# Performance work log

Hardware: AMD Instinct MI355X
Metric: run time of the kernel (lower is better)

The kernel has to match this reference:

```python
import jax, jax.numpy as jnp
import numpy as np

EPS = 1e-5  # BatchNorm eps

def _bn(x):
    # BatchNorm1d(affine=False) in training mode: per-agent, per-feature batch stats
    m = jnp.mean(x, axis=1, keepdims=True)
    v = jnp.var(x, axis=1, keepdims=True)
    return (x - m) / jnp.sqrt(v + EPS)

def _lrelu(x):
    return jax.nn.leaky_relu(x, 0.01)

def setup_inputs() -> dict:
    key = jax.random.key(0)
    ks = jax.random.split(key, 14)
    A, B, IN, OUT, H, K = 8, 32768, 128, 32, 128, 4
    D = H // K
    s = 0.05
    return {
        "states": jax.random.normal(ks[0], (A, B, IN), jnp.float32),
        "actions": jax.random.normal(ks[1], (A, B, OUT), jnp.float32),
        "enc_w": jax.random.normal(ks[2], (A, IN + OUT, H), jnp.float32) * s,
        "enc_b": jax.random.normal(ks[3], (A, H), jnp.float32) * s,
        "aenc_w": jax.random.normal(ks[4], (A, OUT, H), jnp.float32) * s,
        "aenc_b": jax.random.normal(ks[5], (A, H), jnp.float32) * s,
        "key_w": jax.random.normal(ks[6], (K, H, D), jnp.float32) * s,
        "sel_w": jax.random.normal(ks[7], (K, H, D), jnp.float32) * s,
        "val_w": jax.random.normal(ks[8], (K, H, D), jnp.float32) * s,
        "val_b": jax.random.normal(ks[9], (K, D), jnp.float32) * s,
        "c1_w": jax.random.normal(ks[10], (A, 2 * H, H), jnp.float32) * s,
        "c1_b": jax.random.normal(ks[11], (A, H), jnp.float32) * s,
        "c2_w": jax.random.normal(ks[12], (A, H, 1), jnp.float32) * s,
        "c2_b": jax.random.normal(ks[13], (A, 1), jnp.float32) * s,
    }

def reference(states, actions, enc_w, enc_b, aenc_w, aenc_b,
              key_w, sel_w, val_w, val_b, c1_w, c1_b, c2_w, c2_b):
    A, B, _ = states.shape
    # per-agent state-action encodings: [A,B,H]
    sa = _bn(jnp.concatenate([states, actions], axis=-1))
    sa_enc = _lrelu(jnp.einsum('abi,aih->abh', sa, enc_w) + enc_b[:, None, :])
    # per-agent action encodings: [A,B,H]
    a_in = _bn(actions)
    a_enc = _lrelu(jnp.einsum('abi,aih->abh', a_in, aenc_w) + aenc_b[:, None, :])
    # per-head keys/values/selectors: [K,A,B,D]
    keys = jnp.einsum('abh,khd->kabd', a_enc, key_w)
    vals = _lrelu(jnp.einsum('abh,khd->kabd', a_enc, val_w) + val_b[:, None, None, :])
    sels = jnp.einsum('abh,khd->kabd', sa_enc, sel_w)
    D = keys.shape[-1]
    # attention logits over other agents: [K,B,A_query,A_key], self excluded
    logits = jnp.einsum('kibd,kjbd->kbij', sels, keys) / jnp.sqrt(jnp.float32(D))
    self_mask = jnp.eye(A, dtype=bool)[None, None]
    probs = jax.nn.softmax(jnp.where(self_mask, -jnp.inf, logits), axis=-1)
    # attended values: [K,A,B,D] -> concat heads -> [A,B,K*D]
    other = jnp.einsum('kbij,kjbd->kibd', probs, vals)
    other_cat = jnp.transpose(other, (1, 2, 0, 3)).reshape(A, B, -1)
    # per-agent critics on [sa_enc, attended]: [A,B,1]
    critic_in = jnp.concatenate([sa_enc, other_cat], axis=-1)
    h = _lrelu(jnp.einsum('abi,aih->abh', critic_in, c1_w) + c1_b[:, None, :])
    q = jnp.einsum('abh,aho->abo', h, c2_w) + c2_b[:, None, :]
    return q
```

## Files before the change

kernel.cpp:

```cpp
#include <hip/hip_runtime.h>
#include <hip/hip_bf16.h>
#include <stdint.h>

#define A_N 8
#define B_N 32768
#define IN_N 128
#define OUT_N 32
#define SAF 160
#define H_N 128
#define D_N 32
#define KD_N 128
#define CIN_N 256
#define CHUNKS 128
#define EPSV 1e-5f

typedef unsigned int u32;
typedef unsigned short u16;
typedef __attribute__((ext_vector_type(8))) short short8;
typedef __attribute__((ext_vector_type(4))) float floatx4;

typedef __attribute__((address_space(1))) void gvoid;
typedef __attribute__((address_space(3))) void lvoid;
__device__ __forceinline__ void glds16(const void* g, void* l){
  __builtin_amdgcn_global_load_lds((gvoid*)g, (lvoid*)l, 16, 0, 0);
}

__device__ __forceinline__ float bf_lo(u32 u){ return __uint_as_float(u << 16); }
__device__ __forceinline__ float bf_hi(u32 u){ return __uint_as_float(u & 0xffff0000u); }
__device__ __forceinline__ float bf2f(u16 b){ return __uint_as_float(((u32)b) << 16); }
__device__ __forceinline__ u16 f2bf(float f){
  u32 u = __float_as_uint(f);
  return (u16)((u + 0x7fffu + ((u >> 16) & 1u)) >> 16);
}
__device__ __forceinline__ float lrelu(float x){ return x > 0.f ? x : 0.01f * x; }

__global__ __launch_bounds__(256) void k_stats(
    const float* __restrict__ states, const float* __restrict__ actions,
    float* __restrict__ part)
{
  int a = blockIdx.y;
  int chunk = blockIdx.x;
  int t = threadIdx.x;
  int r0 = chunk * (B_N / CHUNKS);
  __shared__ float red[512];
  {
    int f = t & 127, half = t >> 7;
    const float* p = states + ((size_t)a * B_N + r0 + half) * IN_N + f;
    float s1 = 0.f, s2 = 0.f;
    for (int it = 0; it < 128; ++it){
      float v = p[(size_t)(2 * it) * IN_N];
      s1 += v; s2 += v * v;
    }
    red[t] = s1; red[256 + t] = s2;
    __syncthreads();
    if (t < 128){
      float a1 = red[t] + red[t + 128];
      float a2 = red[256 + t] + red[256 + t + 128];
      size_t o = (((size_t)a * CHUNKS + chunk) * SAF + t) * 2;
      part[o] = a1; part[o + 1] = a2;
    }
    __syncthreads();
  }
  {
    int f = t & 31, g = t >> 5;
    const float* p = actions + ((size_t)a * B_N + r0 + g) * OUT_N + f;
    float s1 = 0.f, s2 = 0.f;
    for (int it = 0; it < 32; ++it){
      float v = p[(size_t)(8 * it) * OUT_N];
      s1 += v; s2 += v * v;
    }
    red[t] = s1; red[256 + t] = s2;
    __syncthreads();
    if (t < 32){
      float a1 = 0.f, a2 = 0.f;
      #pragma unroll
      for (int gg = 0; gg < 8; ++gg){
        a1 += red[t + 32 * gg];
        a2 += red[256 + t + 32 * gg];
      }
      size_t o = (((size_t)a * CHUNKS + chunk) * SAF + 128 + t) * 2;
      part[o] = a1; part[o + 1] = a2;
    }
  }
}

__global__ void k_finalize(const float* __restrict__ part,
                           float* __restrict__ meanArr, float* __restrict__ istdArr)
{
  int idx = blockIdx.x * blockDim.x + threadIdx.x;
  if (idx >= A_N * SAF) return;
  int a = idx / SAF, f = idx % SAF;
  float s1 = 0.f, s2 = 0.f;
  for (int c = 0; c < CHUNKS; ++c){
    size_t o = (((size_t)a * CHUNKS + c) * SAF + f) * 2;
    s1 += part[o]; s2 += part[o + 1];
  }
  float m = s1 * (1.f / B_N);
  float v = s2 * (1.f / B_N) - m * m;
  if (v < 0.f) v = 0.f;
  meanArr[idx] = m;
  istdArr[idx] = rsqrtf(v + EPSV);
}

__device__ __forceinline__ void packpair(float w, u16* __restrict__ dh,
                                         u16* __restrict__ dl, int i){
  u16 h = f2bf(w);
  dh[i] = h;
  dl[i] = f2bf(w - bf2f(h));
}

__global__ __launch_bounds__(256) void k_pack(
    const float* __restrict__ enc_w, const float* __restrict__ aenc_w,
    const float* __restrict__ key_w, const float* __restrict__ sel_w,
    const float* __restrict__ val_w, const float* __restrict__ c1_w,
    u16* __restrict__ encH, u16* __restrict__ encL,
    u16* __restrict__ aencH, u16* __restrict__ aencL,
    u16* __restrict__ keyH, u16* __restrict__ selH, u16* __restrict__ valH,
    u16* __restrict__ c1H, u16* __restrict__ c1L)
{
  int i = blockIdx.x * 256 + threadIdx.x;
  const int S0 = A_N * H_N * SAF;
  const int S1 = A_N * H_N * OUT_N;
  const int S2 = KD_N * H_N;
  const int S5 = A_N * H_N * CIN_N;
  if (i < S0){
    int a = i / (H_N * SAF); int r = i % (H_N * SAF);
    int tile = r >> 12; int rr = r & 4095;
    int n = rr >> 5; int kk = rr & 31;
    int kg = tile * 32 + kk;
    packpair(enc_w[((size_t)a * SAF + kg) * H_N + n], encH, encL, i);
    return;
  }
  i -= S0;
  if (i < S1){
    int a = i >> 12; int rr = i & 4095;
    int n = rr >> 5; int k = rr & 31;
    packpair(aenc_w[((size_t)a * OUT_N + k) * H_N + n], aencH, aencL, i);
    return;
  }
  i -= S1;
  if (i < 3 * S2){
    int which = i / S2; int j = i % S2;
    int tile = j >> 12; int rr = j & 4095;
    int n = rr >> 5; int kk = rr & 31;
    int kg = tile * 32 + kk;
    const float* w = (which == 0) ? key_w : ((which == 1) ? sel_w : val_w);
    u16* dh = (which == 0) ? keyH : ((which == 1) ? selH : valH);
    dh[j] = f2bf(w[(((size_t)(n >> 5)) * H_N + kg) * D_N + (n & 31)]);
    return;
  }
  i -= 3 * S2;
  if (i < S5){
    int a = i >> 15; int r = i & 32767;
    int tile = r >> 12; int rr = r & 4095;
    int n = rr >> 5; int kk = rr & 31;
    int kg = tile * 32 + kk;
    packpair(c1_w[((size_t)a * CIN_N + kg) * H_N + n], c1H, c1L, i);
  }
}
#define PACK_TOTAL (A_N*H_N*SAF + A_N*H_N*OUT_N + 3*KD_N*H_N + A_N*H_N*CIN_N)

__global__ __launch_bounds__(256, 3) void k_enc_sel(
    const float* __restrict__ states, const float* __restrict__ actions,
    const float* __restrict__ mean, const float* __restrict__ istd,
    const u16* __restrict__ encH, const u16* __restrict__ encL,
    const float* __restrict__ enc_b,
    const u16* __restrict__ selH,
    u16* __restrict__ sa_enc, u16* __restrict__ sels)
{
  int a = blockIdx.y; int row0 = blockIdx.x * 128; int t = threadIdx.x;
  int lane = t & 63, wave = t >> 6, l16 = lane & 15, quad = lane >> 4;
  __shared__ __align__(16) u16 S[25600];
  __shared__ __align__(16) float sc[160], sh[160];
  u16* Wh = S;
  u16* Wl = S + 4096;
  u16* Xh = S + 8192;
  u16* Xl = S + 13312;
  u16* T  = S;
  u16* Ws = S + 17408;

  if (t < SAF){
    float m = mean[a * SAF + t], s = istd[a * SAF + t];
    sc[t] = s; sh[t] = -m * s;
  }
  floatx4 acc[2][8];
  #pragma unroll
  for (int mt = 0; mt < 2; ++mt)
    #pragma unroll
    for (int nt = 0; nt < 8; ++nt) acc[mt][nt] = (floatx4){0.f,0.f,0.f,0.f};
  const u16* ebh = encH + (size_t)a * (H_N * SAF);
  const u16* ebl = encL + (size_t)a * (H_N * SAF);
  __syncthreads();

  for (int k0 = 0; k0 < SAF; k0 += 32){
    const u16* th = ebh + (k0 >> 5) * 4096;
    const u16* tl = ebl + (k0 >> 5) * 4096;
    #pragma unroll
    for (int c = t; c < 512; c += 256){
      glds16(th + c * 8, Wh + c * 8);
      glds16(tl + c * 8, Wl + c * 8);
    }
    for (int c = t; c < 1024; c += 256){
      int r = c >> 3, kc = (c & 7) * 4, f = k0 + kc;
      size_t row = (size_t)a * B_N + row0 + r;
      float4 v;
      if (f < IN_N) v = *(const float4*)(states + row * IN_N + f);
      else          v = *(const float4*)(actions + row * OUT_N + (f - IN_N));
      float4 scv = *(const float4*)&sc[f];
      float4 shv = *(const float4*)&sh[f];
      float x0 = fmaf(v.x, scv.x, shv.x), x1 = fmaf(v.y, scv.y, shv.y);
      float x2 = fmaf(v.z, scv.z, shv.z), x3 = fmaf(v.w, scv.w, shv.w);
      u16 h0 = f2bf(x0), h1 = f2bf(x1), h2 = f2bf(x2), h3 = f2bf(x3);
      uint2 hv; hv.x = (u32)h0 | ((u32)h1 << 16); hv.y = (u32)h2 | ((u32)h3 << 16);
      *(uint2*)&Xh[r * 40 + kc] = hv;
      u16 l0 = f2bf(x0 - bf2f(h0)), l1 = f2bf(x1 - bf2f(h1));
      u16 l2 = f2bf(x2 - bf2f(h2)), l3 = f2bf(x3 - bf2f(h3));
      uint2 lv; lv.x = (u32)l0 | ((u32)l1 << 16); lv.y = (u32)l2 | ((u32)l3 << 16);
      *(uint2*)&Xl[r * 40 + kc] = lv;
    }
    __syncthreads();
    {
      short8 ah[2], al[2], bh[8], bl[8];
      #pragma unroll
      for (int mt = 0; mt < 2; ++mt){
        int rr = (wave * 32 + mt * 16 + l16) * 40 + quad * 8;
        ah[mt] = *(const short8*)&Xh[rr];
        al[mt] = *(const short8*)&Xl[rr];
      }
      #pragma unroll
      for (int nt = 0; nt < 8; ++nt){
        int rr = (nt * 16 + l16) * 32 + quad * 8;
        bh[nt] = *(const short8*)&Wh[rr];
        bl[nt] = *(const short8*)&Wl[rr];
      }
      #pragma unroll
      for (int mt = 0; mt < 2; ++mt)
        #pragma unroll
        for (int nt = 0; nt < 8; ++nt){
          acc[mt][nt] = __builtin_amdgcn_mfma_f32_16x16x32_bf16(ah[mt], bh[nt], acc[mt][nt], 0,0,0);
          acc[mt][nt] = __builtin_amdgcn_mfma_f32_16x16x32_bf16(ah[mt], bl[nt], acc[mt][nt], 0,0,0);
          acc[mt][nt] = __builtin_amdgcn_mfma_f32_16x16x32_bf16(al[mt], bh[nt], acc[mt][nt], 0,0,0);
        }
    }
    __syncthreads();
  }

  {
    float bv[8];
    #pragma unroll
    for (int nt = 0; nt < 8; ++nt) bv[nt] = enc_b[a * H_N + nt * 16 + l16];
    #pragma unroll
    for (int mt = 0; mt < 2; ++mt)
      #pragma unroll
      for (int nt = 0; nt < 8; ++nt)
        #pragma unroll
        for (int r = 0; r < 4; ++r){
          int rl = wave * 32 + mt * 16 + quad * 4 + r;
          T[rl * 136 + nt * 16 + l16] = f2bf(lrelu(acc[mt][nt][r] + bv[nt]));
        }
  }
  __syncthreads();
  for (int c = t; c < 2048; c += 256){
    int row = c >> 4, col8 = (c & 15) * 8;
    *(uint4*)(sa_enc + ((size_t)a * B_N + row0 + row) * H_N + col8) =
        *(const uint4*)&T[row * 136 + col8];
  }

  #pragma unroll
  for (int mt = 0; mt < 2; ++mt)
    #pragma unroll
    for (int nt = 0; nt < 8; ++nt) acc[mt][nt] = (floatx4){0.f,0.f,0.f,0.f};
  for (int k0 = 0; k0 < H_N; k0 += 64){
    #pragma unroll
    for (int c = t; c < 1024; c += 256)
      glds16(selH + (k0 >> 5) * 4096 + c * 8, Ws + c * 8);
    __syncthreads();
    #pragma unroll
    for (int ks = 0; ks < 64; ks += 32){
      short8 ah[2], bh[8];
      #pragma unroll
      for (int mt = 0; mt < 2; ++mt)
        ah[mt] = *(const short8*)&T[(wave * 32 + mt * 16 + l16) * 136 + k0 + ks + quad * 8];
      #pragma unroll
      for (int nt = 0; nt < 8; ++nt)
        bh[nt] = *(const short8*)&Ws[((ks >> 5) << 12) + (nt * 16 + l16) * 32 + quad * 8];
      #pragma unroll
      for (int mt = 0; mt < 2; ++mt)
        #pragma unroll
        for (int nt = 0; nt < 8; ++nt)
          acc[mt][nt] = __builtin_amdgcn_mfma_f32_16x16x32_bf16(ah[mt], bh[nt], acc[mt][nt], 0,0,0);
    }
    __syncthreads();
  }
  #pragma unroll
  for (int mt = 0; mt < 2; ++mt)
    #pragma unroll
    for (int nt = 0; nt < 8; ++nt)
      #pragma unroll
      for (int r = 0; r < 4; ++r){
        int rl = wave * 32 + mt * 16 + quad * 4 + r;
        T[rl * 136 + nt * 16 + l16] = f2bf(acc[mt][nt][r]);
      }
  __syncthreads();
  for (int c = t; c < 2048; c += 256){
    int row = c >> 4, col8 = (c & 15) * 8;
    *(uint4*)(sels + ((size_t)a * B_N + row0 + row) * H_N + col8) =
        *(const uint4*)&T[row * 136 + col8];
  }
}

__global__ __launch_bounds__(256, 2) void k_aenc_kv(
    const float* __restrict__ actions,
    const float* __restrict__ mean, const float* __restrict__ istd,
    const u16* __restrict__ aencH, const u16* __restrict__ aencL,
    const float* __restrict__ aenc_b,
    const u16* __restrict__ keyH, const u16* __restrict__ valH,
    const float* __restrict__ val_b,
    u16* __restrict__ keys, u16* __restrict__ vals)
{
  int a = blockIdx.y; int row0 = blockIdx.x * 128; int t = threadIdx.x;
  int lane = t & 63, wave = t >> 6, l16 = lane & 15, quad = lane >> 4;
  __shared__ __align__(16) u16 S[34816];
  __shared__ __align__(16) float sc[32], sh[32];
  u16* T  = S;
  u16* WK = S + 17408;
  u16* WV = S + 25600;
  u16* T2 = S + 17408;

  if (t < 32){
    float m = mean[a * SAF + 128 + t], s = istd[a * SAF + 128 + t];
    sc[t] = s; sh[t] = -m * s;
  }
  floatx4 accK[2][8], accV[2][8];
  #pragma unroll
  for (int mt = 0; mt < 2; ++mt)
    #pragma unroll
    for (int nt = 0; nt < 8; ++nt){
      accK[mt][nt] = (floatx4){0.f,0.f,0.f,0.f};
      accV[mt][nt] = (floatx4){0.f,0.f,0.f,0.f};
    }
  __syncthreads();

  {
    u16* Wh1 = S;  u16* Wl1 = S + 4096;
    u16* Xh = S + 8192; u16* Xl = S + 13312;
    const u16* abh = aencH + (size_t)a * 4096;
    const u16* abl = aencL + (size_t)a * 4096;
    #pragma unroll
    for (int c = t; c < 512; c += 256){
      glds16(abh + c * 8, Wh1 + c * 8);
      glds16(abl + c * 8, Wl1 + c * 8);
    }
    for (int c = t; c < 1024; c += 256){
      int r = c >> 3, kc = (c & 7) * 4;
      size_t row = (size_t)a * B_N + row0 + r;
      float4 v = *(const float4*)(actions + row * OUT_N + kc);
      float4 scv = *(const float4*)&sc[kc];
      float4 shv = *(const float4*)&sh[kc];
      float x0 = fmaf(v.x, scv.x, shv.x), x1 = fmaf(v.y, scv.y, shv.y);
      float x2 = fmaf(v.z, scv.z, shv.z), x3 = fmaf(v.w, scv.w, shv.w);
      u16 h0 = f2bf(x0), h1 = f2bf(x1), h2 = f2bf(x2), h3 = f2bf(x3);
      uint2 hv; hv.x = (u32)h0 | ((u32)h1 << 16); hv.y = (u32)h2 | ((u32)h3 << 16);
      *(uint2*)&Xh[r * 40 + kc] = hv;
      u16 l0 = f2bf(x0 - bf2f(h0)), l1 = f2bf(x1 - bf2f(h1));
      u16 l2 = f2bf(x2 - bf2f(h2)), l3 = f2bf(x3 - bf2f(h3));
      uint2 lv; lv.x = (u32)l0 | ((u32)l1 << 16); lv.y = (u32)l2 | ((u32)l3 << 16);
      *(uint2*)&Xl[r * 40 + kc] = lv;
    }
    __syncthreads();
    short8 ah[2], al[2], bh[8], bl[8];
    #pragma unroll
    for (int mt = 0; mt < 2; ++mt){
      int rr = (wave * 32 + mt * 16 + l16) * 40 + quad * 8;
      ah[mt] = *(const short8*)&Xh[rr];
      al[mt] = *(const short8*)&Xl[rr];
    }
    #pragma unroll
    for (int nt = 0; nt < 8; ++nt){
      int rr = (nt * 16 + l16) * 32 + quad * 8;
      bh[nt] = *(const short8*)&Wh1[rr];
      bl[nt] = *(const short8*)&Wl1[rr];
    }
    #pragma unroll
    for (int mt = 0; mt < 2; ++mt)
      #pragma unroll
      for (int nt = 0; nt < 8; ++nt){
        accK[mt][nt] = __builtin_amdgcn_mfma_f32_16x16x32_bf16(ah[mt], bh[nt], accK[mt][nt], 0,0,0);
        accK[mt][nt] = __builtin_amdgcn_mfma_f32_16x16x32_bf16(ah[mt], bl[nt], accK[mt][nt], 0,0,0);
        accK[mt][nt] = __builtin_amdgcn_mfma_f32_16x16x32_bf16(al[mt], bh[nt], accK[mt][nt], 0,0,0);
      }
    __syncthreads();
  }
  {
    float bv[8];
    #pragma unroll
    for (int nt = 0; nt < 8; ++nt) bv[nt] = aenc_b[a * H_N + nt * 16 + l16];
    #pragma unroll
    for (int mt = 0; mt < 2; ++mt)
      #pragma unroll
      for (int nt = 0; nt < 8; ++nt){
        #pragma unroll
        for (int r = 0; r < 4; ++r){
          int rl = wave * 32 + mt * 16 + quad * 4 + r;
          T[rl * 136 + nt * 16 + l16] = f2bf(lrelu(accK[mt][nt][r] + bv[nt]));
        }
        accK[mt][nt] = (floatx4){0.f,0.f,0.f,0.f};
      }
  }

  for (int k0 = 0; k0 < H_N; k0 += 64){
    __syncthreads();
    #pragma unroll
    for (int c = t; c < 1024; c += 256){
      glds16(keyH + (k0 >> 5) * 4096 + c * 8, WK + c * 8);
      glds16(valH + (k0 >> 5) * 4096 + c * 8, WV + c * 8);
    }
    __syncthreads();
    #pragma unroll
    for (int ks = 0; ks < 64; ks += 32){
      short8 ah[2], bk[8], bv[8];
      #pragma unroll
      for (int mt = 0; mt < 2; ++mt)
        ah[mt] = *(const short8*)&T[(wave * 32 + mt * 16 + l16) * 136 + k0 + ks + quad * 8];
      #pragma unroll
      for (int nt = 0; nt < 8; ++nt){
        int rr = ((ks >> 5) << 12) + (nt * 16 + l16) * 32 + quad * 8;
        bk[nt] = *(const short8*)&WK[rr];
        bv[nt] = *(const short8*)&WV[rr];
      }
      #pragma unroll
      for (int mt = 0; mt < 2; ++mt)
        #pragma unroll
        for (int nt = 0; nt < 8; ++nt){
          accK[mt][nt] = __builtin_amdgcn_mfma_f32_16x16x32_bf16(ah[mt], bk[nt], accK[mt][nt], 0,0,0);
          accV[mt][nt] = __builtin_amdgcn_mfma_f32_16x16x32_bf16(ah[mt], bv[nt], accV[mt][nt], 0,0,0);
        }
    }
  }
  __syncthreads();
  {
    float bv[8];
    #pragma unroll
    for (int nt = 0; nt < 8; ++nt) bv[nt] = val_b[nt * 16 + l16];
    #pragma unroll
    for (int mt = 0; mt < 2; ++mt)
      #pragma unroll
      for (int nt = 0; nt < 8; ++nt)
        #pragma unroll
        for (int r = 0; r < 4; ++r){
          int rl = wave * 32 + mt * 16 + quad * 4 + r;
          T[rl * 136 + nt * 16 + l16]  = f2bf(lrelu(accV[mt][nt][r] + bv[nt]));
          T2[rl * 136 + nt * 16 + l16] = f2bf(accK[mt][nt][r]);
        }
  }
  __syncthreads();
  for (int c = t; c < 2048; c += 256){
    int row = c >> 4, col8 = (c & 15) * 8;
    *(uint4*)(vals + ((size_t)a * B_N + row0 + row) * H_N + col8) =
        *(const uint4*)&T[row * 136 + col8];
    *(uint4*)(keys + ((size_t)a * B_N + row0 + row) * H_N + col8) =
        *(const uint4*)&T2[row * 136 + col8];
  }
}

__global__ __launch_bounds__(256) void k_attn(
    const u16* __restrict__ sels, const u16* __restrict__ keys,
    const u16* __restrict__ vals, u16* __restrict__ other)
{
  int b0 = blockIdx.x * 8;
  int t = threadIdx.x;
  __shared__ __align__(16) u16 sS[8192], sK[8192], sV[8192];
  {
    uint4* dS4 = (uint4*)sS; uint4* dK4 = (uint4*)sK; uint4* dV4 = (uint4*)sV;
    #pragma unroll
    for (int c = t; c < 1024; c += 256){
      int aa = c >> 7, o = c & 127;
      size_t go = ((size_t)aa * B_N + b0) * KD_N;
      dS4[c] = *((const uint4*)(sels + go) + o);
      dK4[c] = *((const uint4*)(keys + go) + o);
      dV4[c] = *((const uint4*)(vals + go) + o);
    }
  }
  __syncthreads();
  int i = t & 7, p = t >> 3;
  int k = p & 3, bl = p >> 2;
  int base_i = (i * 8 + bl) * 128 + k * 32;
  float si[32];
  {
    const u32* S32 = (const u32*)&sS[base_i];
    #pragma unroll
    for (int d2 = 0; d2 < 16; ++d2){
      u32 u = S32[d2];
      si[2 * d2] = bf_lo(u); si[2 * d2 + 1] = bf_hi(u);
    }
  }
  float lg[8];
  #pragma unroll
  for (int j = 0; j < 8; ++j){
    const u32* K32 = (const u32*)&sK[(j * 8 + bl) * 128 + k * 32];
    float acc = 0.f;
    #pragma unroll
    for (int d2 = 0; d2 < 16; ++d2){
      u32 u = K32[d2];
      acc = fmaf(si[2 * d2], bf_lo(u), acc);
      acc = fmaf(si[2 * d2 + 1], bf_hi(u), acc);
    }
    lg[j] = acc * 0.17677669529663689f;
  }
  float mx = -3.0e38f;
  #pragma unroll
  for (int j = 0; j < 8; ++j) if (j != i) mx = fmaxf(mx, lg[j]);
  float pe[8], se = 0.f;
  #pragma unroll
  for (int j = 0; j < 8; ++j){
    pe[j] = (j == i) ? 0.f : __expf(lg[j] - mx);
    se += pe[j];
  }
  float inv = 1.f / se;
  #pragma unroll
  for (int j = 0; j < 8; ++j) pe[j] *= inv;
  __align__(16) u16 ob[32];
  #pragma unroll
  for (int d2 = 0; d2 < 16; ++d2){
    float acc0 = 0.f, acc1 = 0.f;
    #pragma unroll
    for (int j = 0; j < 8; ++j){
      u32 u = *(const u32*)&sV[(j * 8 + bl) * 128 + k * 32 + 2 * d2];
      acc0 = fmaf(pe[j], bf_lo(u), acc0);
      acc1 = fmaf(pe[j], bf_hi(u), acc1);
    }
    ob[2 * d2] = f2bf(acc0); ob[2 * d2 + 1] = f2bf(acc1);
  }
  uint4* dst = (uint4*)(other + ((size_t)i * B_N + (b0 + bl)) * KD_N + k * 32);
  const uint4* s4 = (const uint4*)ob;
  #pragma unroll
  for (int c = 0; c < 4; ++c) dst[c] = s4[c];
}

__global__ __launch_bounds__(256, 3) void k_critic(
    const u16* __restrict__ sa_enc, const u16* __restrict__ other,
    const u16* __restrict__ c1H, const u16* __restrict__ c1L,
    const float* __restrict__ c1_b,
    const float* __restrict__ c2w, const float* __restrict__ c2b,
    float* __restrict__ qout)
{
  int a = blockIdx.y; int row0 = blockIdx.x * 128; int t = threadIdx.x;
  int lane = t & 63, wave = t >> 6, l16 = lane & 15, quad = lane >> 4;
  __shared__ __align__(16) u16 Xs[4096];
  __shared__ __align__(16) u16 Wh[4096];
  __shared__ __align__(16) u16 Wl[4096];
  floatx4 acc[2][8];
  #pragma unroll
  for (int mt = 0; mt < 2; ++mt)
    #pragma unroll
    for (int nt = 0; nt < 8; ++nt) acc[mt][nt] = (floatx4){0.f,0.f,0.f,0.f};
  const u16* wbh = c1H + (size_t)a * (H_N * CIN_N);
  const u16* wbl = c1L + (size_t)a * (H_N * CIN_N);

  for (int k0 = 0; k0 < CIN_N; k0 += 32){
    const u16* th = wbh + (k0 >> 5) * 4096;
    const u16* tl = wbl + (k0 >> 5) * 4096;
    #pragma unroll
    for (int c = t; c < 512; c += 256){
      glds16(th + c * 8, Wh + c * 8);
      glds16(tl + c * 8, Wl + c * 8);
    }
    {
      const u16* src = (k0 < H_N) ? sa_enc : other;
      int kb = (k0 < H_N) ? k0 : k0 - H_N;
      #pragma unroll
      for (int c = t; c < 512; c += 256){
        int r = c >> 2, off = (c & 3) * 8;
        glds16(src + ((size_t)a * B_N + row0 + r) * H_N + kb + off, Xs + c * 8);
      }
    }
    __syncthreads();
    {
      short8 ah[2], bh[8], bl[8];
      #pragma unroll
      for (int mt = 0; mt < 2; ++mt)
        ah[mt] = *(const short8*)&Xs[(wave * 32 + mt * 16 + l16) * 32 + quad * 8];
      #pragma unroll
      for (int nt = 0; nt < 8; ++nt){
        int rr = (nt * 16 + l16) * 32 + quad * 8;
        bh[nt] = *(const short8*)&Wh[rr];
        bl[nt] = *(const short8*)&Wl[rr];
      }
      #pragma unroll
      for (int mt = 0; mt < 2; ++mt)
        #pragma unroll
        for (int nt = 0; nt < 8; ++nt){
          acc[mt][nt] = __builtin_amdgcn_mfma_f32_16x16x32_bf16(ah[mt], bh[nt], acc[mt][nt], 0,0,0);
          acc[mt][nt] = __builtin_amdgcn_mfma_f32_16x16x32_bf16(ah[mt], bl[nt], acc[mt][nt], 0,0,0);
        }
    }
    __syncthreads();
  }

  float c2r[8], bv[8];
  #pragma unroll
  for (int nt = 0; nt < 8; ++nt){
    c2r[nt] = c2w[a * H_N + nt * 16 + l16];
    bv[nt]  = c1_b[a * H_N + nt * 16 + l16];
  }
  #pragma unroll
  for (int mt = 0; mt < 2; ++mt){
    #pragma unroll
    for (int r = 0; r < 4; ++r){
      float s = 0.f;
      #pragma unroll
      for (int nt = 0; nt < 8; ++nt){
        float h = lrelu(acc[mt][nt][r] + bv[nt]);
        s = fmaf(h, c2r[nt], s);
      }
      s += __shfl_xor(s, 1);
      s += __shfl_xor(s, 2);
      s += __shfl_xor(s, 4);
      s += __shfl_xor(s, 8);
      if (l16 == 0){
        int row = row0 + wave * 32 + mt * 16 + quad * 4 + r;
        qout[(size_t)a * B_N + row] = s + c2b[a];
      }
    }
  }
}

extern "C" void kernel_launch(void* const* d_in, const int* in_sizes, int n_in,
                              void* d_out, int out_size, void* d_ws, size_t ws_size,
                              hipStream_t stream)
{
  const float* states  = (const float*)d_in[0];
  const float* actions = (const float*)d_in[1];
  const float* enc_w   = (const float*)d_in[2];
  const float* enc_b   = (const float*)d_in[3];
  const float* aenc_w  = (const float*)d_in[4];
  const float* aenc_b  = (const float*)d_in[5];
  const float* key_w   = (const float*)d_in[6];
  const float* sel_w   = (const float*)d_in[7];
  const float* val_w   = (const float*)d_in[8];
  const float* val_b   = (const float*)d_in[9];
  const float* c1_w    = (const float*)d_in[10];
  const float* c1_b    = (const float*)d_in[11];
  const float* c2_w    = (const float*)d_in[12];
  const float* c2_b    = (const float*)d_in[13];
  float* q = (float*)d_out;

  char* ws = (char*)d_ws;
  u16* encH  = (u16*)(ws + 0);
  u16* encL  = (u16*)(ws + 327680);
  u16* aencH = (u16*)(ws + 655360);
  u16* aencL = (u16*)(ws + 720896);
  u16* keyH  = (u16*)(ws + 786432);
  u16* selH  = (u16*)(ws + 819200);
  u16* valH  = (u16*)(ws + 851968);
  float* part    = (float*)ws;
  float* meanArr = (float*)(ws + 1310720);
  float* istdArr = (float*)(ws + 1315840);
  u16* c1H = (u16*)(ws + 1320960);
  u16* c1L = (u16*)(ws + 1845248);
  const size_t ibase = 4194304;
  const size_t BUF = (size_t)A_N * B_N * 128 * 2;
  u16* sa_enc = (u16*)(ws + ibase);
  u16* sels   = (u16*)(ws + ibase + BUF);
  u16* keys   = (u16*)(ws + ibase + 2 * BUF);
  u16* vals   = (u16*)(ws + ibase + 3 * BUF);

  k_stats<<<dim3(CHUNKS, A_N), 256, 0, stream>>>(states, actions, part);
  k_finalize<<<(A_N * SAF + 255) / 256, 256, 0, stream>>>(part, meanArr, istdArr);
  k_pack<<<(PACK_TOTAL + 255) / 256, 256, 0, stream>>>(
      enc_w, aenc_w, key_w, sel_w, val_w, c1_w,
      encH, encL, aencH, aencL, keyH, selH, valH, c1H, c1L);

  dim3 g(B_N / 128, A_N);
  k_enc_sel<<<g, 256, 0, stream>>>(states, actions, meanArr, istdArr,
                                   encH, encL, enc_b, selH, sa_enc, sels);
  k_aenc_kv<<<g, 256, 0, stream>>>(actions, meanArr, istdArr,
                                   aencH, aencL, aenc_b, keyH, valH, val_b,
                                   keys, vals);
  k_attn<<<B_N / 8, 256, 0, stream>>>(sels, keys, vals, keys);
  k_critic<<<g, 256, 0, stream>>>(sa_enc, keys, c1H, c1L, c1_b, c2_w, c2_b, q);
}
```

Before: 509.8 us.

## Swizzle LDS tiles, prefetch next K-tiles, and double-buffer critic GEMM loads

Applies an XOR swizzle to the LDS weight and activation tiles in the encoder, key/value and critic kernels to cut bank conflicts on short8 MFMA operand reads. Prefetches the next states/actions chunk into registers and issues the next weight tile's global-to-LDS loads right after the compute barrier, using explicit waitcnt and raw barriers instead of __syncthreads. The critic kernel gets a double-buffered LDS pipeline so global loads overlap MFMA work. The attention kernel stages sels/keys/vals in a swizzled layout read as uint4 vectors. The hand-written waitcnt counts must match the number of outstanding loads, and double buffering raises LDS use per block, which may lower occupancy.

```diff
diff --git a/kernel.cpp b/kernel.cpp
--- a/kernel.cpp
+++ b/kernel.cpp
@@ -23,6 +23,14 @@
 typedef __attribute__((address_space(3))) void lvoid;
 __device__ __forceinline__ void glds16(const void* g, void* l){
   __builtin_amdgcn_global_load_lds((gvoid*)g, (lvoid*)l, 16, 0, 0);
+}
+
+__device__ __forceinline__ int swzu(int u){ return u ^ ((u >> 3) & 3); }
+
+__device__ __forceinline__ void hard_barrier(){
+  asm volatile("" ::: "memory");
+  __builtin_amdgcn_s_barrier();
+  asm volatile("" ::: "memory");
 }
 
 __device__ __forceinline__ float bf_lo(u32 u){ return __uint_as_float(u << 16); }
@@ -192,20 +200,28 @@
   const u16* ebl = encL + (size_t)a * (H_N * SAF);
   __syncthreads();
 
-  for (int k0 = 0; k0 < SAF; k0 += 32){
-    const u16* th = ebh + (k0 >> 5) * 4096;
-    const u16* tl = ebl + (k0 >> 5) * 4096;
-    #pragma unroll
-    for (int c = t; c < 512; c += 256){
-      glds16(th + c * 8, Wh + c * 8);
-      glds16(tl + c * 8, Wl + c * 8);
-    }
-    for (int c = t; c < 1024; c += 256){
+  float4 xr[4];
+  #pragma unroll
+  for (int ci = 0; ci < 4; ++ci){
+    int c = t + ci * 256;
+    int r = c >> 3, kc = (c & 7) * 4;
+    xr[ci] = *(const float4*)(states + ((size_t)a * B_N + row0 + r) * IN_N + kc);
+  }
+  #pragma unroll
+  for (int c = t; c < 512; c += 256){
+    glds16(ebh + swzu(c) * 8, Wh + c * 8);
+    glds16(ebl + swzu(c) * 8, Wl + c * 8);
+  }
+  asm volatile("" ::: "memory");
+
+  #pragma unroll
+  for (int kt = 0; kt < 5; ++kt){
+    int k0 = kt * 32;
+    #pragma unroll
+    for (int ci = 0; ci < 4; ++ci){
+      int c = t + ci * 256;
       int r = c >> 3, kc = (c & 7) * 4, f = k0 + kc;
-      size_t row = (size_t)a * B_N + row0 + r;
-      float4 v;
-      if (f < IN_N) v = *(const float4*)(states + row * IN_N + f);
-      else          v = *(const float4*)(actions + row * OUT_N + (f - IN_N));
+      float4 v = xr[ci];
       float4 scv = *(const float4*)&sc[f];
       float4 shv = *(const float4*)&sh[f];
       float x0 = fmaf(v.x, scv.x, shv.x), x1 = fmaf(v.y, scv.y, shv.y);
@@ -218,7 +234,21 @@
       uint2 lv; lv.x = (u32)l0 | ((u32)l1 << 16); lv.y = (u32)l2 | ((u32)l3 << 16);
       *(uint2*)&Xl[r * 40 + kc] = lv;
     }
-    __syncthreads();
+    if (kt < 4){
+      #pragma unroll
+      for (int ci = 0; ci < 4; ++ci){
+        int c = t + ci * 256;
+        int r = c >> 3, kc = (c & 7) * 4;
+        size_t row = (size_t)a * B_N + row0 + r;
+        if (kt < 3) xr[ci] = *(const float4*)(states + row * IN_N + (kt + 1) * 32 + kc);
+        else        xr[ci] = *(const float4*)(actions + row * OUT_N + kc);
+      }
+      asm volatile("s_waitcnt vmcnt(4) lgkmcnt(0)" ::: "memory");
+    } else {
+      asm volatile("s_waitcnt vmcnt(0) lgkmcnt(0)" ::: "memory");
+    }
+    __builtin_amdgcn_s_barrier();
+    asm volatile("" ::: "memory");
     {
       short8 ah[2], al[2], bh[8], bl[8];
       #pragma unroll
@@ -229,9 +259,9 @@
       }
       #pragma unroll
       for (int nt = 0; nt < 8; ++nt){
-        int rr = (nt * 16 + l16) * 32 + quad * 8;
-        bh[nt] = *(const short8*)&Wh[rr];
-        bl[nt] = *(const short8*)&Wl[rr];
+        int v = (nt * 16 + l16) * 4 + quad; v ^= (v >> 3) & 3;
+        bh[nt] = *(const short8*)&Wh[v * 8];
+        bl[nt] = *(const short8*)&Wl[v * 8];
       }
       #pragma unroll
       for (int mt = 0; mt < 2; ++mt)
@@ -242,7 +272,17 @@
           acc[mt][nt] = __builtin_amdgcn_mfma_f32_16x16x32_bf16(al[mt], bh[nt], acc[mt][nt], 0,0,0);
         }
     }
-    __syncthreads();
+    hard_barrier();
+    if (kt < 4){
+      const u16* th = ebh + (kt + 1) * 4096;
+      const u16* tl = ebl + (kt + 1) * 4096;
+      #pragma unroll
+      for (int c = t; c < 512; c += 256){
+        glds16(th + swzu(c) * 8, Wh + c * 8);
+        glds16(tl + swzu(c) * 8, Wl + c * 8);
+      }
+      asm volatile("" ::: "memory");
+    }
   }
 
   {
@@ -260,21 +300,25 @@
         }
   }
   __syncthreads();
+  #pragma unroll
+  for (int c = t; c < 1024; c += 256)
+    glds16(selH + swzu(c) * 8, Ws + c * 8);
+  asm volatile("" ::: "memory");
   for (int c = t; c < 2048; c += 256){
     int row = c >> 4, col8 = (c & 15) * 8;
     *(uint4*)(sa_enc + ((size_t)a * B_N + row0 + row) * H_N + col8) =
         *(const uint4*)&T[row * 136 + col8];
   }
-
   #pragma unroll
   for (int mt = 0; mt < 2; ++mt)
     #pragma unroll
     for (int nt = 0; nt < 8; ++nt) acc[mt][nt] = (floatx4){0.f,0.f,0.f,0.f};
+
+  asm volatile("s_waitcnt vmcnt(0)" ::: "memory");
+  __builtin_amdgcn_s_barrier();
+  asm volatile("" ::: "memory");
+  #pragma unroll
   for (int k0 = 0; k0 < H_N; k0 += 64){
-    #pragma unroll
-    for (int c = t; c < 1024; c += 256)
-      glds16(selH + (k0 >> 5) * 4096 + c * 8, Ws + c * 8);
-    __syncthreads();
     #pragma unroll
     for (int ks = 0; ks < 64; ks += 32){
       short8 ah[2], bh[8];
@@ -282,15 +326,25 @@
       for (int mt = 0; mt < 2; ++mt)
         ah[mt] = *(const short8*)&T[(wave * 32 + mt * 16 + l16) * 136 + k0 + ks + quad * 8];
       #pragma unroll
-      for (int nt = 0; nt < 8; ++nt)
-        bh[nt] = *(const short8*)&Ws[((ks >> 5) << 12) + (nt * 16 + l16) * 32 + quad * 8];
+      for (int nt = 0; nt < 8; ++nt){
+        int v = ((ks >> 5) << 9) + (nt * 16 + l16) * 4 + quad; v ^= (v >> 3) & 3;
+        bh[nt] = *(const short8*)&Ws[v * 8];
+      }
       #pragma unroll
       for (int mt = 0; mt < 2; ++mt)
         #pragma unroll
         for (int nt = 0; nt < 8; ++nt)
           acc[mt][nt] = __builtin_amdgcn_mfma_f32_16x16x32_bf16(ah[mt], bh[nt], acc[mt][nt], 0,0,0);
     }
-    __syncthreads();
+    hard_barrier();
+    if (k0 == 0){
+      #pragma unroll
+      for (int c = t; c < 1024; c += 256)
+        glds16(selH + 8192 + swzu(c) * 8, Ws + c * 8);
+      asm volatile("s_waitcnt vmcnt(0)" ::: "memory");
+      __builtin_amdgcn_s_barrier();
+      asm volatile("" ::: "memory");
+    }
   }
   #pragma unroll
   for (int mt = 0; mt < 2; ++mt)
@@ -348,8 +402,8 @@
     const u16* abl = aencL + (size_t)a * 4096;
     #pragma unroll
     for (int c = t; c < 512; c += 256){
-      glds16(abh + c * 8, Wh1 + c * 8);
-      glds16(abl + c * 8, Wl1 + c * 8);
+      glds16(abh + swzu(c) * 8, Wh1 + c * 8);
+      glds16(abl + swzu(c) * 8, Wl1 + c * 8);
     }
     for (int c = t; c < 1024; c += 256){
       int r = c >> 3, kc = (c & 7) * 4;
@@ -377,9 +431,9 @@
     }
     #pragma unroll
     for (int nt = 0; nt < 8; ++nt){
-      int rr = (nt * 16 + l16) * 32 + quad * 8;
-      bh[nt] = *(const short8*)&Wh1[rr];
-      bl[nt] = *(const short8*)&Wl1[rr];
+      int v = (nt * 16 + l16) * 4 + quad; v ^= (v >> 3) & 3;
+      bh[nt] = *(const short8*)&Wh1[v * 8];
+      bl[nt] = *(const short8*)&Wl1[v * 8];
     }
     #pragma unroll
     for (int mt = 0; mt < 2; ++mt)
@@ -412,8 +466,8 @@
     __syncthreads();
     #pragma unroll
     for (int c = t; c < 1024; c += 256){
-      glds16(keyH + (k0 >> 5) * 4096 + c * 8, WK + c * 8);
-      glds16(valH + (k0 >> 5) * 4096 + c * 8, WV + c * 8);
+      glds16(keyH + (k0 >> 5) * 4096 + swzu(c) * 8, WK + c * 8);
+      glds16(valH + (k0 >> 5) * 4096 + swzu(c) * 8, WV + c * 8);
     }
     __syncthreads();
     #pragma unroll
@@ -424,9 +478,9 @@
         ah[mt] = *(const short8*)&T[(wave * 32 + mt * 16 + l16) * 136 + k0 + ks + quad * 8];
       #pragma unroll
       for (int nt = 0; nt < 8; ++nt){
-        int rr = ((ks >> 5) << 12) + (nt * 16 + l16) * 32 + quad * 8;
-        bk[nt] = *(const short8*)&WK[rr];
-        bv[nt] = *(const short8*)&WV[rr];
+        int v = ((ks >> 5) << 9) + (nt * 16 + l16) * 4 + quad; v ^= (v >> 3) & 3;
+        bk[nt] = *(const short8*)&WK[v * 8];
+        bv[nt] = *(const short8*)&WV[v * 8];
       }
       #pragma unroll
       for (int mt = 0; mt < 2; ++mt)
@@ -470,40 +524,46 @@
   int b0 = blockIdx.x * 8;
   int t = threadIdx.x;
   __shared__ __align__(16) u16 sS[8192], sK[8192], sV[8192];
-  {
-    uint4* dS4 = (uint4*)sS; uint4* dK4 = (uint4*)sK; uint4* dV4 = (uint4*)sV;
-    #pragma unroll
-    for (int c = t; c < 1024; c += 256){
-      int aa = c >> 7, o = c & 127;
-      size_t go = ((size_t)aa * B_N + b0) * KD_N;
-      dS4[c] = *((const uint4*)(sels + go) + o);
-      dK4[c] = *((const uint4*)(keys + go) + o);
-      dV4[c] = *((const uint4*)(vals + go) + o);
-    }
+  #pragma unroll
+  for (int c = t; c < 1024; c += 256){
+    int pr = c >> 4, uir = c & 15;
+    int aa = pr & 7, bl2 = pr >> 3;
+    int kk = uir >> 2, dg = uir & 3;
+    int U = (bl2 * 4 + dg) * 32 + kk * 8 + (aa ^ (kk << 1));
+    size_t go = ((size_t)aa * B_N + b0 + bl2) * KD_N;
+    ((uint4*)sS)[U] = *((const uint4*)(sels + go) + uir);
+    ((uint4*)sK)[U] = *((const uint4*)(keys + go) + uir);
+    ((uint4*)sV)[U] = *((const uint4*)(vals + go) + uir);
   }
   __syncthreads();
-  int i = t & 7, p = t >> 3;
-  int k = p & 3, bl = p >> 2;
-  int base_i = (i * 8 + bl) * 128 + k * 32;
+  int i = t & 7, k = (t >> 3) & 3, bl = t >> 5;
   float si[32];
-  {
-    const u32* S32 = (const u32*)&sS[base_i];
-    #pragma unroll
-    for (int d2 = 0; d2 < 16; ++d2){
-      u32 u = S32[d2];
-      si[2 * d2] = bf_lo(u); si[2 * d2 + 1] = bf_hi(u);
+  #pragma unroll
+  for (int dg = 0; dg < 4; ++dg){
+    int U = (bl * 4 + dg) * 32 + k * 8 + (i ^ (k << 1));
+    uint4 s4 = ((const uint4*)sS)[U];
+    const u32* sp = (const u32*)&s4;
+    #pragma unroll
+    for (int jj = 0; jj < 4; ++jj){
+      int d2 = dg * 4 + jj;
+      si[2 * d2] = bf_lo(sp[jj]); si[2 * d2 + 1] = bf_hi(sp[jj]);
     }
   }
   float lg[8];
   #pragma unroll
   for (int j = 0; j < 8; ++j){
-    const u32* K32 = (const u32*)&sK[(j * 8 + bl) * 128 + k * 32];
     float acc = 0.f;
     #pragma unroll
-    for (int d2 = 0; d2 < 16; ++d2){
-      u32 u = K32[d2];
-      acc = fmaf(si[2 * d2], bf_lo(u), acc);
-      acc = fmaf(si[2 * d2 + 1], bf_hi(u), acc);
+    for (int dg = 0; dg < 4; ++dg){
+      int U = (bl * 4 + dg) * 32 + k * 8 + (j ^ (k << 1));
+      uint4 k4 = ((const uint4*)sK)[U];
+      const u32* kp = (const u32*)&k4;
+      #pragma unroll
+      for (int jj = 0; jj < 4; ++jj){
+        int d2 = dg * 4 + jj;
+        acc = fmaf(si[2 * d2], bf_lo(kp[jj]), acc);
+        acc = fmaf(si[2 * d2 + 1], bf_hi(kp[jj]), acc);
+      }
     }
     lg[j] = acc * 0.17677669529663689f;
   }
@@ -519,22 +579,33 @@
   float inv = 1.f / se;
   #pragma unroll
   for (int j = 0; j < 8; ++j) pe[j] *= inv;
+  float o0[16], o1[16];
+  #pragma unroll
+  for (int d2 = 0; d2 < 16; ++d2){ o0[d2] = 0.f; o1[d2] = 0.f; }
+  #pragma unroll
+  for (int j = 0; j < 8; ++j){
+    #pragma unroll
+    for (int dg = 0; dg < 4; ++dg){
+      int U = (bl * 4 + dg) * 32 + k * 8 + (j ^ (k << 1));
+      uint4 v4 = ((const uint4*)sV)[U];
+      const u32* vp = (const u32*)&v4;
+      #pragma unroll
+      for (int jj = 0; jj < 4; ++jj){
+        int d2 = dg * 4 + jj;
+        o0[d2] = fmaf(pe[j], bf_lo(vp[jj]), o0[d2]);
+        o1[d2] = fmaf(pe[j], bf_hi(vp[jj]), o1[d2]);
+      }
+    }
+  }
   __align__(16) u16 ob[32];
   #pragma unroll
   for (int d2 = 0; d2 < 16; ++d2){
-    float acc0 = 0.f, acc1 = 0.f;
-    #pragma unroll
-    for (int j = 0; j < 8; ++j){
-      u32 u = *(const u32*)&sV[(j * 8 + bl) * 128 + k * 32 + 2 * d2];
-      acc0 = fmaf(pe[j], bf_lo(u), acc0);
-      acc1 = fmaf(pe[j], bf_hi(u), acc1);
-    }
-    ob[2 * d2] = f2bf(acc0); ob[2 * d2 + 1] = f2bf(acc1);
+    ob[2 * d2] = f2bf(o0[d2]); ob[2 * d2 + 1] = f2bf(o1[d2]);
   }
   uint4* dst = (uint4*)(other + ((size_t)i * B_N + (b0 + bl)) * KD_N + k * 32);
-  const uint4* s4 = (const uint4*)ob;
-  #pragma unroll
-  for (int c = 0; c < 4; ++c) dst[c] = s4[c];
+  const uint4* s4o = (const uint4*)ob;
+  #pragma unroll
+  for (int c = 0; c < 4; ++c) dst[c] = s4o[c];
 }
 
 __global__ __launch_bounds__(256, 3) void k_critic(
@@ -546,9 +617,7 @@
 {
   int a = blockIdx.y; int row0 = blockIdx.x * 128; int t = threadIdx.x;
   int lane = t & 63, wave = t >> 6, l16 = lane & 15, quad = lane >> 4;
-  __shared__ __align__(16) u16 Xs[4096];
-  __shared__ __align__(16) u16 Wh[4096];
-  __shared__ __align__(16) u16 Wl[4096];
+  __shared__ __align__(16) u16 Buf[2][12288];
   floatx4 acc[2][8];
   #pragma unroll
   for (int mt = 0; mt < 2; ++mt)
@@ -557,34 +626,48 @@
   const u16* wbh = c1H + (size_t)a * (H_N * CIN_N);
   const u16* wbl = c1L + (size_t)a * (H_N * CIN_N);
 
-  for (int k0 = 0; k0 < CIN_N; k0 += 32){
-    const u16* th = wbh + (k0 >> 5) * 4096;
-    const u16* tl = wbl + (k0 >> 5) * 4096;
+  auto stage = [&](int kt, int b){
+    const u16* th = wbh + kt * 4096;
+    const u16* tl = wbl + kt * 4096;
+    const u16* src = (kt < 4) ? sa_enc : other;
+    int kb = (kt < 4) ? kt * 32 : kt * 32 - H_N;
+    u16* Xs = Buf[b]; u16* Wh = Buf[b] + 4096; u16* Wl = Buf[b] + 8192;
     #pragma unroll
     for (int c = t; c < 512; c += 256){
-      glds16(th + c * 8, Wh + c * 8);
-      glds16(tl + c * 8, Wl + c * 8);
-    }
+      glds16(th + swzu(c) * 8, Wh + c * 8);
+      glds16(tl + swzu(c) * 8, Wl + c * 8);
+      int r = c >> 2, q = (c & 3) ^ ((c >> 3) & 3);
+      glds16(src + ((size_t)a * B_N + row0 + r) * H_N + kb + q * 8, Xs + c * 8);
+    }
+  };
+
+  stage(0, 0);
+  asm volatile("" ::: "memory");
+  #pragma unroll
+  for (int kt = 0; kt < 8; ++kt){
+    if (kt < 7){
+      stage(kt + 1, (kt + 1) & 1);
+      asm volatile("s_waitcnt vmcnt(6)" ::: "memory");
+    } else {
+      asm volatile("s_waitcnt vmcnt(0)" ::: "memory");
+    }
+    __builtin_amdgcn_s_barrier();
+    asm volatile("" ::: "memory");
     {
-      const u16* src = (k0 < H_N) ? sa_enc : other;
-      int kb = (k0 < H_N) ? k0 : k0 - H_N;
-      #pragma unroll
-      for (int c = t; c < 512; c += 256){
-        int r = c >> 2, off = (c & 3) * 8;
-        glds16(src + ((size_t)a * B_N + row0 + r) * H_N + kb + off, Xs + c * 8);
-      }
-    }
-    __syncthreads();
-    {
+      const u16* Xs = Buf[kt & 1];
+      const u16* Wh = Buf[kt & 1] + 4096;
+      const u16* Wl = Buf[kt & 1] + 8192;
       short8 ah[2], bh[8], bl[8];
       #pragma unroll
-      for (int mt = 0; mt < 2; ++mt)
-        ah[mt] = *(const short8*)&Xs[(wave * 32 + mt * 16 + l16) * 32 + quad * 8];
+      for (int mt = 0; mt < 2; ++mt){
+        int v = (wave * 32 + mt * 16 + l16) * 4 + quad; v ^= (v >> 3) & 3;
+        ah[mt] = *(const short8*)&Xs[v * 8];
+      }
       #pragma unroll
       for (int nt = 0; nt < 8; ++nt){
-        int rr = (nt * 16 + l16) * 32 + quad * 8;
-        bh[nt] = *(const short8*)&Wh[rr];
-        bl[nt] = *(const short8*)&Wl[rr];
+        int v = (nt * 16 + l16) * 4 + quad; v ^= (v >> 3) & 3;
+        bh[nt] = *(const short8*)&Wh[v * 8];
+        bl[nt] = *(const short8*)&Wl[v * 8];
       }
       #pragma unroll
       for (int mt = 0; mt < 2; ++mt)
@@ -594,7 +677,7 @@
           acc[mt][nt] = __builtin_amdgcn_mfma_f32_16x16x32_bf16(ah[mt], bl[nt], acc[mt][nt], 0,0,0);
         }
     }
-    __syncthreads();
+    hard_barrier();
   }
 
   float c2r[8], bv[8];
```

New measurement: 558.7 us. +9.6%, slower.
